# Kernel tuning notes

Measured on AMD Instinct MI355X. Metric: run time of the kernel, lower is better.

Reference implementation:

```python
import jax, jax.numpy as jnp
from jax import lax
import numpy as np


def _conv(x, w, b, stride=1, pad=0):
    # x: NCHW, w: OIHW
    o = lax.conv_general_dilated(x, w, (stride, stride), [(pad, pad), (pad, pad)],
                                 dimension_numbers=('NCHW', 'OIHW', 'NCHW'))
    return o + b[None, :, None, None]


def _up2(x):
    return jnp.repeat(jnp.repeat(x, 2, axis=2), 2, axis=3)


def _boundary_agg(x, w, b):
    # up_to_bottom = prefix-max along H; bottom_to_up = suffix-max along H;
    # left_to_right / right_to_left (via rot90) = prefix/suffix max along W (square spatial).
    x1 = lax.cummax(x, axis=2)
    x2 = lax.cummax(x, axis=2, reverse=True)
    x3 = lax.cummax(x, axis=3)
    x4 = lax.cummax(x, axis=3, reverse=True)
    return _conv(jnp.concatenate([x, x1, x2, x3, x4], axis=1), w, b)


def _forward(C3, C4, C5,
             ba3_w, ba3_b, ba4_w, ba4_b, ba5_w, ba5_b,
             p5_1_w, p5_1_b, p5_1d_w, p5_1d_b, p5_2_w, p5_2_b,
             p4_1_w, p4_1_b, p4_1d_w, p4_1d_b, p4_2_w, p4_2_b,
             p3_1_w, p3_1_b, p3_1d_w, p3_1d_b, p3_2_w, p3_2_b,
             p6_w, p6_b, p7_w, p7_b,
             c34_w, c34_b, c45_w, c45_b, c35_w, c35_b,
             gamma3, gamma4, gamma5):
    C3_BA = _boundary_agg(C3, ba3_w, ba3_b)
    C4_BA = _boundary_agg(C4, ba4_w, ba4_b)
    C5_BA = _boundary_agg(C5, ba5_w, ba5_b)
    # top-down path
    P5 = _conv(C5, p5_1_w, p5_1_b)
    P5u1 = _up2(P5)
    P5u2 = _up2(P5u1)
    P5 = _conv(P5, p5_2_w, p5_2_b, 1, 1)
    P4 = _conv(C4, p4_1_w, p4_1_b) + P5u1
    P4u1 = _up2(P4)
    P4 = _conv(P4, p4_2_w, p4_2_b, 1, 1)
    P3 = _conv(C3, p3_1_w, p3_1_b) + P4u1 + P5u2
    P3 = _conv(P3, p3_2_w, p3_2_b, 1, 1)
    # bottom-up (dual) path on boundary-aggregated features
    P3d = _conv(C3_BA, p3_1d_w, p3_1d_b)
    P3d1 = _conv(P3d, c34_w, c34_b, 2, 1)   # 3x3 s2 p1
    P3d2 = _conv(P3d1, c35_w, c35_b, 2, 0)  # 2x2 s2 p0
    P4d = _conv(C4_BA, p4_1d_w, p4_1d_b) + P3d1
    P4d1 = _conv(P4d, c45_w, c45_b, 2, 0)   # 2x2 s2 p0
    P5d = _conv(C5_BA, p5_1d_w, p5_1d_b) + P4d1 + P3d2
    # extra levels
    P6 = _conv(C5, p6_w, p6_b, 2, 1)
    P7 = _conv(jax.nn.relu(P6), p7_w, p7_b, 2, 1)
    # gated merge
    O3 = gamma3 * P3d + (1.0 - gamma3) * P3
    O4 = gamma4 * P4d + (1.0 - gamma4) * P4
    O5 = gamma5 * P5d + (1.0 - gamma5) * P5
    return (O3, O4, O5, P6, P7)


def setup_inputs() -> dict:
    key = jax.random.key(0)
    ks = iter(jax.random.split(key, 48))
    def rnd(shape, scale):
        return jax.random.normal(next(ks), shape, dtype=jnp.float32) * scale
    B, F = 8, 256
    d = {
        'C3': rnd((B, 256, 64, 64), 1.0),
        'C4': rnd((B, 512, 32, 32), 1.0),
        'C5': rnd((B, 1024, 16, 16), 1.0),
        # Boundary_Aggregation 1x1 convs: in_channels*5 -> in_channels
        'ba3_w': rnd((256, 1280, 1, 1), 0.02), 'ba3_b': rnd((256,), 0.02),
        'ba4_w': rnd((512, 2560, 1, 1), 0.02), 'ba4_b': rnd((512,), 0.02),
        'ba5_w': rnd((1024, 5120, 1, 1), 0.01), 'ba5_b': rnd((1024,), 0.02),
        # FPN lateral / smoothing convs
        'p5_1_w': rnd((F, 1024, 1, 1), 0.02), 'p5_1_b': rnd((F,), 0.02),
        'p5_1d_w': rnd((F, 1024, 1, 1), 0.02), 'p5_1d_b': rnd((F,), 0.02),
        'p5_2_w': rnd((F, F, 3, 3), 0.02), 'p5_2_b': rnd((F,), 0.02),
        'p4_1_w': rnd((F, 512, 1, 1), 0.02), 'p4_1_b': rnd((F,), 0.02),
        'p4_1d_w': rnd((F, 512, 1, 1), 0.02), 'p4_1d_b': rnd((F,), 0.02),
        'p4_2_w': rnd((F, F, 3, 3), 0.02), 'p4_2_b': rnd((F,), 0.02),
        'p3_1_w': rnd((F, 256, 1, 1), 0.02), 'p3_1_b': rnd((F,), 0.02),
        'p3_1d_w': rnd((F, 256, 1, 1), 0.02), 'p3_1d_b': rnd((F,), 0.02),
        'p3_2_w': rnd((F, F, 3, 3), 0.02), 'p3_2_b': rnd((F,), 0.02),
        'p6_w': rnd((F, 1024, 3, 3), 0.02), 'p6_b': rnd((F,), 0.02),
        'p7_w': rnd((F, F, 3, 3), 0.02), 'p7_b': rnd((F,), 0.02),
        # downsample convs in dual path
        'c34_w': rnd((F, F, 3, 3), 0.02), 'c34_b': rnd((F,), 0.02),
        'c45_w': rnd((F, F, 2, 2), 0.02), 'c45_b': rnd((F,), 0.02),
        'c35_w': rnd((F, F, 2, 2), 0.02), 'c35_b': rnd((F,), 0.02),
        'gamma3': rnd((1,), 0.3), 'gamma4': rnd((1,), 0.3), 'gamma5': rnd((1,), 0.3),
    }
    return d


def reference(C3, C4, C5,
              ba3_w, ba3_b, ba4_w, ba4_b, ba5_w, ba5_b,
              p5_1_w, p5_1_b, p5_1d_w, p5_1d_b, p5_2_w, p5_2_b,
              p4_1_w, p4_1_b, p4_1d_w, p4_1d_b, p4_2_w, p4_2_b,
              p3_1_w, p3_1_b, p3_1d_w, p3_1d_b, p3_2_w, p3_2_b,
              p6_w, p6_b, p7_w, p7_b,
              c34_w, c34_b, c45_w, c45_b, c35_w, c35_b,
              gamma3, gamma4, gamma5):
    return _forward(C3, C4, C5,
                    ba3_w, ba3_b, ba4_w, ba4_b, ba5_w, ba5_b,
                    p5_1_w, p5_1_b, p5_1d_w, p5_1d_b, p5_2_w, p5_2_b,
                    p4_1_w, p4_1_b, p4_1d_w, p4_1d_b, p4_2_w, p4_2_b,
                    p3_1_w, p3_1_b, p3_1d_w, p3_1d_b, p3_2_w, p3_2_b,
                    p6_w, p6_b, p7_w, p7_b,
                    c34_w, c34_b, c45_w, c45_b, c35_w, c35_b,
                    gamma3, gamma4, gamma5)
```

## Files before the change

### kernel.cpp

```cpp
#include <hip/hip_runtime.h>

typedef unsigned short u16;
typedef __attribute__((ext_vector_type(8))) short s8v;
typedef __attribute__((ext_vector_type(4))) float f4v;

__device__ __forceinline__ u16 f2bf(float f) {
  unsigned int x = __float_as_uint(f);
  return (u16)((x + 0x7fffu + ((x >> 16) & 1u)) >> 16);
}
__device__ __forceinline__ float bf2f(u16 u) {
  return __uint_as_float(((unsigned int)u) << 16);
}
__device__ __forceinline__ void gload16(const void* g, void* l) {
  __builtin_amdgcn_global_load_lds(
      (const __attribute__((address_space(1))) void*)g,
      (__attribute__((address_space(3))) void*)l, 16, 0, 0);
}

struct Epi {
  const float* bias;
  const u16* r1; int r1Hp, r1pad, r1sh;
  const u16* r2; int r2Hp, r2pad, r2sh;
  const float* gamma; const u16* other; int oHp, opad, gmode;
  u16* outB; int oBHp, oBpad, oBrelu;
  float* outF;
};

__device__ __forceinline__ size_t nhwc_idx(int b, int h, int w, int Hp, int pad, int Cc, int m) {
  return (((size_t)(b * Hp + h + pad)) * Hp + (w + pad)) * Cc + m;
}

__device__ __forceinline__ void epi4(f4v a, int mbase, int b, int oh, int ow,
                                     int p, int M, int l2ohow, float g, const Epi& ep) {
  float v[4];
#pragma unroll
  for (int r = 0; r < 4; ++r) v[r] = a[r];
  if (ep.bias) {
    const float* bp = &ep.bias[mbase];
#pragma unroll
    for (int r = 0; r < 4; ++r) v[r] += bp[r];
  }
  if (ep.r1) {
    const u16* rp = &ep.r1[nhwc_idx(b, oh >> ep.r1sh, ow >> ep.r1sh, ep.r1Hp, ep.r1pad, 256, mbase)];
#pragma unroll
    for (int r = 0; r < 4; ++r) v[r] += bf2f(rp[r]);
  }
  if (ep.r2) {
    const u16* rp = &ep.r2[nhwc_idx(b, oh >> ep.r2sh, ow >> ep.r2sh, ep.r2Hp, ep.r2pad, 256, mbase)];
#pragma unroll
    for (int r = 0; r < 4; ++r) v[r] += bf2f(rp[r]);
  }
  if (ep.gmode) {
    const u16* op = &ep.other[nhwc_idx(b, oh, ow, ep.oHp, ep.opad, 256, mbase)];
#pragma unroll
    for (int r = 0; r < 4; ++r) {
      float o = bf2f(op[r]);
      v[r] = (ep.gmode == 1) ? (g * o + (1.f - g) * v[r]) : (g * v[r] + (1.f - g) * o);
    }
  }
  if (ep.outF) {
    float* fp = &ep.outF[(((size_t)(b * M + mbase)) << l2ohow) + p];
#pragma unroll
    for (int r = 0; r < 4; ++r) fp[(size_t)r << l2ohow] = v[r];
  }
  if (ep.outB) {
    u16* obp = &ep.outB[nhwc_idx(b, oh, ow, ep.oBHp, ep.oBpad, M, mbase)];
    ushort4 pk;
    if (ep.oBrelu) { pk.x = f2bf(fmaxf(v[0], 0.f)); pk.y = f2bf(fmaxf(v[1], 0.f));
                     pk.z = f2bf(fmaxf(v[2], 0.f)); pk.w = f2bf(fmaxf(v[3], 0.f)); }
    else { pk.x = f2bf(v[0]); pk.y = f2bf(v[1]); pk.z = f2bf(v[2]); pk.w = f2bf(v[3]); }
    *(ushort4*)obp = pk;
  }
}

struct WSeg { const float* src; u16* dst; int K, l2Cin, mode, ktiles, blk0; };
struct WTab { WSeg s[17]; };

__global__ __launch_bounds__(256) void k_cvt_w(WTab tab) {
  int bid = blockIdx.x;
  int si = 0;
#pragma unroll
  for (int i = 1; i < 17; ++i) si += (bid >= tab.s[i].blk0) ? 1 : 0;
  WSeg sg = tab.s[si];
  int rel = bid - sg.blk0;
  int m = rel / sg.ktiles;
  int kt = rel - m * sg.ktiles;
  int r = kt * 256 + threadIdx.x;
  if (r >= sg.K) return;
  int Cin = 1 << sg.l2Cin;
  int q = r >> sg.l2Cin, c = r & (Cin - 1);
  int sidx;
  if (sg.mode == 1) {
    int og = (q < 4) ? (q + 1) : 0;
    sidx = m * sg.K + og * Cin + c;
  } else {
    int KHW = sg.K >> sg.l2Cin;
    sidx = (m * Cin + c) * KHW + q;
  }
  sg.dst[(size_t)m * sg.K + r] = f2bf(sg.src[sidx]);
}

__global__ __launch_bounds__(256) void k_cvt_x(const float* __restrict__ in, u16* __restrict__ out,
                                               int C, int H, int W, int Hp, int P, int tw) {
  __shared__ u16 tile[32][33];
  const int t = threadIdx.x;
  const int b = blockIdx.z, h = blockIdx.y;
  const int tc = blockIdx.x / tw, twi = blockIdx.x - tc * tw;
  const int c0 = tc * 32, w0 = twi * 32;
#pragma unroll
  for (int r = 0; r < 4; ++r) {
    int cl = (t >> 5) * 4 + r, wl = t & 31;
    if (w0 + wl < W) tile[cl][wl] = f2bf(in[(((size_t)b * C + c0 + cl) * H + h) * W + w0 + wl]);
  }
  __syncthreads();
#pragma unroll
  for (int r = 0; r < 4; ++r) {
    int wl = (t >> 5) * 4 + r, cl = t & 31;
    if (w0 + wl < W) out[(((size_t)(b * Hp + h + P)) * Hp + (w0 + wl + P)) * C + c0 + cl] = tile[cl][wl];
  }
}

template<int S, int L2S>
__global__ __launch_bounds__(256) void k_scan2(const float* __restrict__ x,
                                               u16* __restrict__ out, int l2C) {
  __shared__ u16 pl[S][S + 1], rp[S][S + 1], rs[S][S + 1];
  const int pid = blockIdx.x;
  const size_t SS = (size_t)S * S;
  const size_t GS = ((size_t)8 << l2C) * SS;
  const float* xp = x + (size_t)pid * SS;
  u16* g0 = out + (size_t)pid * SS;
  u16* g1 = g0 + GS;
  u16* g2 = g1 + GS;
  u16* g3 = g2 + GS;
  const int t = threadIdx.x;
  for (int idx = t; idx < S * S; idx += 256)
    pl[idx >> L2S][idx & (S - 1)] = f2bf(xp[idx]);
  __syncthreads();
  if (t < S) {
    float m = -INFINITY;
    for (int h = 0; h < S; ++h) { m = fmaxf(m, bf2f(pl[h][t])); g0[h * S + t] = f2bf(m); }
  } else if (t < 2 * S) {
    int c = t - S;
    float m = -INFINITY;
    for (int h = S - 1; h >= 0; --h) { m = fmaxf(m, bf2f(pl[h][c])); g1[h * S + c] = f2bf(m); }
  } else if (t < 3 * S) {
    int h = t - 2 * S;
    float m = -INFINITY;
    for (int w = 0; w < S; ++w) { m = fmaxf(m, bf2f(pl[h][w])); rp[h][w] = f2bf(m); }
  } else if (t < 4 * S) {
    int h = t - 3 * S;
    float m = -INFINITY;
    for (int w = S - 1; w >= 0; --w) { m = fmaxf(m, bf2f(pl[h][w])); rs[h][w] = f2bf(m); }
  }
  __syncthreads();
  for (int idx = t; idx < S * S; idx += 256) {
    g2[idx] = rp[idx >> L2S][idx & (S - 1)];
    g3[idx] = rs[idx >> L2S][idx & (S - 1)];
  }
}

__global__ __launch_bounds__(256) void k_tr(const u16* __restrict__ src, u16* __restrict__ dst,
                                            int C, int S, int tw) {
  __shared__ u16 tile[32][33];
  const int t = threadIdx.x;
  const int z = blockIdx.z, h = blockIdx.y;
  const int tc = blockIdx.x / tw, twi = blockIdx.x - tc * tw;
  const int c0 = tc * 32, w0 = twi * 32;
  const size_t SS = (size_t)S * S;
  const u16* sp = src + (size_t)z * C * SS;
  u16* dp = dst + (size_t)z * SS * C;
#pragma unroll
  for (int r = 0; r < 4; ++r) {
    int cl = (t >> 5) * 4 + r, wl = t & 31;
    if (w0 + wl < S) tile[cl][wl] = sp[(size_t)(c0 + cl) * SS + h * S + w0 + wl];
  }
  __syncthreads();
#pragma unroll
  for (int r = 0; r < 4; ++r) {
    int wl = (t >> 5) * 4 + r, cl = t & 31;
    if (w0 + wl < S) dp[((size_t)(h * S + w0 + wl)) * C + c0 + cl] = tile[cl][wl];
  }
}

template<int QDIV, int KW, int STR, bool FUSE>
__global__ __launch_bounds__(256)
void k_gemm(const u16* __restrict__ X, const u16* __restrict__ X2,
            const u16* __restrict__ Wt,
            float* __restrict__ part, int C, int l2C, int Hp, int ipad,
            int l2ohow, int l2ow, int K, int Ksp, int M, int N, Epi ep) {
  __shared__ u16 Al[4096];
  __shared__ u16 Bl[8192];
  const int tid = threadIdx.x, lane = tid & 63, wid = tid >> 6;

  int ntile, mtile;
  {
    const int NT = gridDim.x, MT = gridDim.y;
    int nm = blockIdx.x + NT * blockIdx.y;
    if ((NT & 7) == 0) {
      int low = nm & 7, r = nm >> 3;
      mtile = r % MT;
      ntile = ((r / MT) << 3) + low;
    } else { ntile = blockIdx.x; mtile = blockIdx.y; }
  }
  const int n0 = ntile * 128, m0 = mtile * 64;
  const int kb = blockIdx.z * Ksp;
  const int mw = (wid >> 1) * 32, nw = (wid & 1) * 64;

  const int srow = lane >> 2;
  const int schunk = (lane & 3) ^ ((srow >> 1) & 3);

  const u16* pa0 = Wt + (size_t)(m0 + wid * 16 + srow) * K + kb + schunk * 8;

  const u16* pb0 = nullptr; const u16* pb1 = nullptr;
  int rowB[2], ohsB[2], owsB[2];
  int q = 0, cnt = 0, khs = 0, kws = 0;
#pragma unroll
  for (int j = 0; j < 2; ++j) {
    int n = n0 + wid * 32 + j * 16 + srow;
    int b = n >> l2ohow, p = n & ((1 << l2ohow) - 1);
    int oh = p >> l2ow, ow = p & ((1 << l2ow) - 1);
    if (QDIV == 1) {
      const u16* gg = X + ((size_t)(b * Hp + oh + ipad) * Hp + (ow + ipad)) * C + kb + schunk * 8;
      if (j == 0) pb0 = gg; else pb1 = gg;
    } else if (QDIV == 5) {
      rowB[j] = n;
    } else {
      rowB[j] = b * Hp; ohsB[j] = oh * STR + ipad; owsB[j] = ow * STR + ipad;
    }
  }
  if (QDIV == 5) {
    q = kb >> l2C;
    int c0 = kb & (C - 1);
    cnt = (C - c0) >> 5;
    const u16* base = (q < 4) ? (X + (((size_t)q << Hp) << l2C)) : X2;
    pb0 = base + (((size_t)rowB[0]) << l2C) + c0 + schunk * 8;
    pb1 = base + (((size_t)rowB[1]) << l2C) + c0 + schunk * 8;
  } else if (QDIV != 1) {
    q = kb >> l2C;
    int c0 = kb & (C - 1);
    cnt = (C - c0) >> 5;
    if (QDIV == 4) { khs = q >> 1; kws = q & 1; } else { khs = q / 3; kws = q - khs * 3; }
    pb0 = X + ((size_t)(rowB[0] + ohsB[0] + khs) * Hp + (owsB[0] + kws)) * C + c0 + schunk * 8;
    pb1 = X + ((size_t)(rowB[1] + ohsB[1] + khs) * Hp + (owsB[1] + kws)) * C + c0 + schunk * 8;
  }

  f4v acc[2][4];
#pragma unroll
  for (int i = 0; i < 2; ++i)
#pragma unroll
    for (int j = 0; j < 4; ++j) acc[i][j] = (f4v){0.f, 0.f, 0.f, 0.f};

  const int fr = lane & 15, kc = lane >> 4;
  const int fxor = (kc ^ ((fr >> 1) & 3)) * 8;

  auto advB = [&]() {
    if (QDIV == 1) { pb0 += 32; pb1 += 32; }
    else if (--cnt == 0) {
      ++q; cnt = C >> 5;
      if (QDIV == 5) {
        const u16* base = (q < 4) ? (X + (((size_t)q << Hp) << l2C)) : X2;
        pb0 = base + (((size_t)rowB[0]) << l2C) + schunk * 8;
        pb1 = base + (((size_t)rowB[1]) << l2C) + schunk * 8;
      } else {
        if (++kws == KW) { kws = 0; ++khs; }
        pb0 = X + ((size_t)(rowB[0] + ohsB[0] + khs) * Hp + (owsB[0] + kws)) * C + schunk * 8;
        pb1 = X + ((size_t)(rowB[1] + ohsB[1] + khs) * Hp + (owsB[1] + kws)) * C + schunk * 8;
      }
    } else { pb0 += 32; pb1 += 32; }
  };
  auto stage = [&](int buf) {
    u16* la = Al + buf * 2048 + wid * 512;
    u16* lb = Bl + buf * 4096 + wid * 1024;
    gload16(pa0, la);
    gload16(pb0, lb); gload16(pb1, lb + 512);
    pa0 += 32;
    advB();
  };

  const int nt = Ksp >> 5;
  stage(0);
  for (int t = 0; t < nt; ++t) {
    const int cur = t & 1;
    if (t + 1 < nt) {
      stage(cur ^ 1);
      asm volatile("s_waitcnt vmcnt(3)" ::: "memory");
    } else {
      asm volatile("s_waitcnt vmcnt(0)" ::: "memory");
    }
    __builtin_amdgcn_s_barrier();
    asm volatile("" ::: "memory");
    const u16* ca = Al + cur * 2048;
    const u16* cb = Bl + cur * 4096;
    s8v a[2], bv[4];
#pragma unroll
    for (int mf = 0; mf < 2; ++mf) a[mf] = *(const s8v*)&ca[(mw + mf * 16 + fr) * 32 + fxor];
#pragma unroll
    for (int nf = 0; nf < 4; ++nf) bv[nf] = *(const s8v*)&cb[(nw + nf * 16 + fr) * 32 + fxor];
#pragma unroll
    for (int mf = 0; mf < 2; ++mf)
#pragma unroll
      for (int nf = 0; nf < 4; ++nf)
        acc[mf][nf] = __builtin_amdgcn_mfma_f32_16x16x32_bf16(a[mf], bv[nf], acc[mf][nf], 0, 0, 0);
    __builtin_amdgcn_s_barrier();
    asm volatile("" ::: "memory");
  }

  const int r4 = kc * 4;
  if (FUSE) {
    float g = ep.gmode ? *ep.gamma : 0.f;
#pragma unroll
    for (int nf = 0; nf < 4; ++nf) {
      int n = n0 + nw + nf * 16 + fr;
      int b = n >> l2ohow, p = n & ((1 << l2ohow) - 1);
      int oh = p >> l2ow, ow = p & ((1 << l2ow) - 1);
#pragma unroll
      for (int mf = 0; mf < 2; ++mf)
        epi4(acc[mf][nf], m0 + mw + mf * 16 + r4, b, oh, ow, p, M, l2ohow, g, ep);
    }
  } else {
#pragma unroll
    for (int nf = 0; nf < 4; ++nf) {
      int n = n0 + nw + nf * 16 + fr;
      float* pr = part + ((size_t)blockIdx.z * N + n) * M + m0 + mw + r4;
#pragma unroll
      for (int mf = 0; mf < 2; ++mf)
        *(f4v*)&pr[mf * 16] = acc[mf][nf];
    }
  }
}

__global__ __launch_bounds__(256)
void k_red2(const float* __restrict__ part, int z, int l2N, int l2M4, int M,
            int l2ohow, int l2ow, Epi ep) {
  const size_t total = (size_t)1 << (l2N + l2M4);
  const int N = 1 << l2N;
  float g = ep.gmode ? *ep.gamma : 0.f;
  for (size_t t = (size_t)blockIdx.x * 256 + threadIdx.x; t < total;
       t += (size_t)gridDim.x * 256) {
    int m4 = (int)(t & ((1u << l2M4) - 1));
    int n = (int)(t >> l2M4);
    int m = m4 << 2;
    f4v v = (f4v){0.f, 0.f, 0.f, 0.f};
    for (int s = 0; s < z; ++s) {
      f4v x = *(const f4v*)&part[((size_t)s * N + n) * M + m];
      v = v + x;
    }
    int b = n >> l2ohow, p = n & ((1 << l2ohow) - 1);
    int oh = p >> l2ow, ow = p & ((1 << l2ow) - 1);
    epi4(v, m, b, oh, ow, p, M, l2ohow, g, ep);
  }
}

static const size_t WR_BA3 = 0, WR_BA4 = 327680, WR_BA5 = 1638400,
  WR_P51 = 6881280, WR_P51D = 7143424, WR_P52 = 7405568, WR_P41 = 7995392,
  WR_P41D = 8126464, WR_P42 = 8257536, WR_P31 = 8847360, WR_P31D = 8912896,
  WR_P32 = 8978432, WR_P6 = 9568256, WR_P7 = 11927552, WR_C34 = 12517376,
  WR_C45 = 13107200, WR_C35 = 13369344;
static const size_t O_C3N = 13631488, O_C4N = 22020096, O_C5N = 26214400,
  O_C3BA = 28311552, O_C4BA = 36700160, O_C5BA = 40894464,
  O_CAT = 42991616, O_SCR = 76546048;
static const size_t O_P3D = O_CAT, O_P3PRE = O_CAT + 8921088,
  O_P4PRE = O_CAT + 17842176, O_P3D1 = O_CAT + 20209664,
  O_P4D = O_CAT + 22306816, O_P4D1 = O_CAT + 24403968,
  O_P3D2 = O_CAT + 24928256, O_P5PRE = O_CAT + 25452544,
  O_P5S = O_CAT + 26116096, O_P6R = O_CAT + 26640384, O_C5P = O_CAT + 26845184;

extern "C" void kernel_launch(void* const* d_in, const int* in_sizes, int n_in,
                              void* d_out, int out_size, void* d_ws, size_t ws_size,
                              hipStream_t stream) {
  (void)in_sizes; (void)n_in; (void)out_size; (void)ws_size;
  const float* C3 = (const float*)d_in[0];
  const float* C4 = (const float*)d_in[1];
  const float* C5 = (const float*)d_in[2];
  const float* ba3_w = (const float*)d_in[3];  const float* ba3_b = (const float*)d_in[4];
  const float* ba4_w = (const float*)d_in[5];  const float* ba4_b = (const float*)d_in[6];
  const float* ba5_w = (const float*)d_in[7];  const float* ba5_b = (const float*)d_in[8];
  const float* p5_1_w = (const float*)d_in[9];  const float* p5_1_b = (const float*)d_in[10];
  const float* p5_1d_w = (const float*)d_in[11]; const float* p5_1d_b = (const float*)d_in[12];
  const float* p5_2_w = (const float*)d_in[13]; const float* p5_2_b = (const float*)d_in[14];
  const float* p4_1_w = (const float*)d_in[15]; const float* p4_1_b = (const float*)d_in[16];
  const float* p4_1d_w = (const float*)d_in[17]; const float* p4_1d_b = (const float*)d_in[18];
  const float* p4_2_w = (const float*)d_in[19]; const float* p4_2_b = (const float*)d_in[20];
  const float* p3_1_w = (const float*)d_in[21]; const float* p3_1_b = (const float*)d_in[22];
  const float* p3_1d_w = (const float*)d_in[23]; const float* p3_1d_b = (const float*)d_in[24];
  const float* p3_2_w = (const float*)d_in[25]; const float* p3_2_b = (const float*)d_in[26];
  const float* p6_w = (const float*)d_in[27]; const float* p6_b = (const float*)d_in[28];
  const float* p7_w = (const float*)d_in[29]; const float* p7_b = (const float*)d_in[30];
  const float* c34_w = (const float*)d_in[31]; const float* c34_b = (const float*)d_in[32];
  const float* c45_w = (const float*)d_in[33]; const float* c45_b = (const float*)d_in[34];
  const float* c35_w = (const float*)d_in[35]; const float* c35_b = (const float*)d_in[36];
  const float* g3 = (const float*)d_in[37];
  const float* g4 = (const float*)d_in[38];
  const float* g5 = (const float*)d_in[39];

  float* out = (float*)d_out;
  float* O3 = out;
  float* O4 = out + 8388608;
  float* O5 = out + 10485760;
  float* P6o = out + 11010048;
  float* P7o = out + 11141120;

  u16* wsu = (u16*)d_ws;
  u16* c3n = wsu + O_C3N;  u16* c4n = wsu + O_C4N;  u16* c5n = wsu + O_C5N;
  u16* c3ba = wsu + O_C3BA; u16* c4ba = wsu + O_C4BA; u16* c5ba = wsu + O_C5BA;
  u16* catb = wsu + O_CAT;
  u16* scr = wsu + O_SCR;
  u16* p3d = wsu + O_P3D;  u16* p3d1 = wsu + O_P3D1; u16* p3d2 = wsu + O_P3D2;
  u16* p4d = wsu + O_P4D;  u16* p4d1 = wsu + O_P4D1;
  u16* p5pre = wsu + O_P5PRE; u16* p5s = wsu + O_P5S; u16* p4pre = wsu + O_P4PRE;
  u16* p3pre = wsu + O_P3PRE; u16* p6r = wsu + O_P6R; u16* c5p = wsu + O_C5P;
  float* part = (float*)scr;
  float* partba = (float*)scr;

  const Epi enone = {nullptr, nullptr,0,0,0, nullptr,0,0,0, nullptr,nullptr,0,0,0, nullptr,0,0,0, nullptr};

  WTab tab;
  int ti = 0, blk = 0;
  auto add = [&](const float* s, size_t off, int M, int K, int l2Cin, int mode) {
    int kt = (K + 255) / 256;
    tab.s[ti].src = s; tab.s[ti].dst = wsu + off; tab.s[ti].K = K;
    tab.s[ti].l2Cin = l2Cin; tab.s[ti].mode = mode;
    tab.s[ti].ktiles = kt; tab.s[ti].blk0 = blk;
    blk += M * kt; ++ti;
  };
  add(ba3_w, WR_BA3, 256, 1280, 8, 1);
  add(ba4_w, WR_BA4, 512, 2560, 9, 1);
  add(ba5_w, WR_BA5, 1024, 5120, 10, 1);
  add(p5_1_w, WR_P51, 256, 1024, 10, 0);
  add(p5_1d_w, WR_P51D, 256, 1024, 10, 0);
  add(p5_2_w, WR_P52, 256, 2304, 8, 0);
  add(p4_1_w, WR_P41, 256, 512, 9, 0);
  add(p4_1d_w, WR_P41D, 256, 512, 9, 0);
  add(p4_2_w, WR_P42, 256, 2304, 8, 0);
  add(p3_1_w, WR_P31, 256, 256, 8, 0);
  add(p3_1d_w, WR_P31D, 256, 256, 8, 0);
  add(p3_2_w, WR_P32, 256, 2304, 8, 0);
  add(p6_w, WR_P6, 256, 9216, 10, 0);
  add(p7_w, WR_P7, 256, 2304, 8, 0);
  add(c34_w, WR_C34, 256, 2304, 8, 0);
  add(c45_w, WR_C45, 256, 1024, 8, 0);
  add(c35_w, WR_C35, 256, 1024, 8, 0);
  k_cvt_w<<<blk, 256, 0, stream>>>(tab);

  k_cvt_x<<<dim3(16,64,8), 256, 0, stream>>>(C3, c3n, 256, 64, 64, 64, 0, 2);
  k_cvt_x<<<dim3(16,32,8), 256, 0, stream>>>(C4, c4n, 512, 32, 32, 32, 0, 1);
  k_cvt_x<<<dim3(32,16,8), 256, 0, stream>>>(C5, c5n, 1024, 16, 16, 16, 0, 1);

  k_scan2<64, 6><<<2048, 256, 0, stream>>>(C3, scr, 8);
  k_tr<<<dim3(16,64,32), 256, 0, stream>>>(scr, catb, 256, 64, 2);
  {
    Epi ep = {ba3_b, nullptr,0,0,0, nullptr,0,0,0, nullptr,nullptr,0,0,0, c3ba,64,0,0, nullptr};
    k_gemm<5,1,1,true><<<dim3(256,4,1), 256, 0, stream>>>(
        catb, c3n, wsu + WR_BA3, nullptr, 256, 8, 15, 0, 12, 6, 1280, 1280, 256, 32768, ep);
  }
  k_scan2<32, 5><<<4096, 256, 0, stream>>>(C4, scr, 9);
  k_tr<<<dim3(16,32,32), 256, 0, stream>>>(scr, catb, 512, 32, 1);
  k_gemm<5,1,1,false><<<dim3(64,8,2), 256, 0, stream>>>(
      catb, c4n, wsu + WR_BA4, partba, 512, 9, 13, 0, 10, 5, 2560, 1280, 512, 8192, enone);
  {
    Epi ep = {ba4_b, nullptr,0,0,0, nullptr,0,0,0, nullptr,nullptr,0,0,0, c4ba,32,0,0, nullptr};
    k_red2<<<2048, 256, 0, stream>>>(partba, 2, 13, 7, 512, 10, 5, ep);
  }
  k_scan2<16, 4><<<8192, 256, 0, stream>>>(C5, scr, 10);
  k_tr<<<dim3(32,16,32), 256, 0, stream>>>(scr, catb, 1024, 16, 1);
  k_gemm<5,1,1,false><<<dim3(16,16,4), 256, 0, stream>>>(
      catb, c5n, wsu + WR_BA5, partba, 1024, 10, 11, 0, 8, 4, 5120, 1280, 1024, 2048, enone);
  {
    Epi ep = {ba5_b, nullptr,0,0,0, nullptr,0,0,0, nullptr,nullptr,0,0,0, c5ba,16,0,0, nullptr};
    k_red2<<<2048, 256, 0, stream>>>(partba, 4, 11, 8, 1024, 8, 4, ep);
  }

  hipMemsetAsync(p3d, 0, (size_t)8921088 * 2, stream);
  hipMemsetAsync(p3pre, 0, (size_t)8921088 * 2, stream);
  hipMemsetAsync(p4pre, 0, (size_t)2367488 * 2, stream);
  hipMemsetAsync(p5pre, 0, (size_t)663552 * 2, stream);
  hipMemsetAsync(p6r, 0, (size_t)204800 * 2, stream);
  hipMemsetAsync(c5p, 0, (size_t)2654208 * 2, stream);
  k_cvt_x<<<dim3(32,16,8), 256, 0, stream>>>(C5, c5p, 1024, 16, 16, 18, 1, 1);

  {
    Epi ep = {p3_1d_b, nullptr,0,0,0, nullptr,0,0,0, nullptr,nullptr,0,0,0, p3d,66,1,0, nullptr};
    k_gemm<1,1,1,true><<<dim3(256,4,1), 256, 0, stream>>>(
        c3ba, nullptr, wsu + WR_P31D, nullptr, 256, 0, 64, 0, 12, 6, 256, 256, 256, 32768, ep);
  }
  k_gemm<9,3,2,false><<<dim3(64,4,4), 256, 0, stream>>>(
      p3d, nullptr, wsu + WR_C34, part, 256, 8, 66, 0, 10, 5, 2304, 576, 256, 8192, enone);
  {
    Epi ep = {c34_b, nullptr,0,0,0, nullptr,0,0,0, nullptr,nullptr,0,0,0, p3d1,32,0,0, nullptr};
    k_red2<<<2048, 256, 0, stream>>>(part, 4, 13, 6, 256, 10, 5, ep);
  }
  k_gemm<4,2,2,false><<<dim3(16,4,8), 256, 0, stream>>>(
      p3d1, nullptr, wsu + WR_C35, part, 256, 8, 32, 0, 8, 4, 1024, 128, 256, 2048, enone);
  {
    Epi ep = {c35_b, nullptr,0,0,0, nullptr,0,0,0, nullptr,nullptr,0,0,0, p3d2,16,0,0, nullptr};
    k_red2<<<2048, 256, 0, stream>>>(part, 8, 11, 6, 256, 8, 4, ep);
  }
  k_gemm<1,1,1,false><<<dim3(64,4,4), 256, 0, stream>>>(
      c4ba, nullptr, wsu + WR_P41D, part, 512, 0, 32, 0, 10, 5, 512, 128, 256, 8192, enone);
  {
    Epi ep = {p4_1d_b, p3d1,32,0,0, nullptr,0,0,0, nullptr,nullptr,0,0,0, p4d,32,0,0, nullptr};
    k_red2<<<2048, 256, 0, stream>>>(part, 4, 13, 6, 256, 10, 5, ep);
  }
  k_gemm<4,2,2,false><<<dim3(16,4,8), 256, 0, stream>>>(
      p4d, nullptr, wsu + WR_C45, part, 256, 8, 32, 0, 8, 4, 1024, 128, 256, 2048, enone);
  {
    Epi ep = {c45_b, nullptr,0,0,0, nullptr,0,0,0, nullptr,nullptr,0,0,0, p4d1,16,0,0, nullptr};
    k_red2<<<2048, 256, 0, stream>>>(part, 8, 11, 6, 256, 8, 4, ep);
  }

  k_gemm<1,1,1,false><<<dim3(16,4,8), 256, 0, stream>>>(
      c5n, nullptr, wsu + WR_P51, part, 1024, 0, 16, 0, 8, 4, 1024, 128, 256, 2048, enone);
  {
    Epi ep = {p5_1_b, nullptr,0,0,0, nullptr,0,0,0, nullptr,nullptr,0,0,0, p5pre,18,1,0, nullptr};
    k_red2<<<2048, 256, 0, stream>>>(part, 8, 11, 6, 256, 8, 4, ep);
  }
  k_gemm<9,3,1,false><<<dim3(16,4,8), 256, 0, stream>>>(
      p5pre, nullptr, wsu + WR_P52, part, 256, 8, 18, 0, 8, 4, 2304, 288, 256, 2048, enone);
  {
    Epi ep = {p5_2_b, nullptr,0,0,0, nullptr,0,0,0, nullptr,nullptr,0,0,0, p5s,16,0,0, nullptr};
    k_red2<<<2048, 256, 0, stream>>>(part, 8, 11, 6, 256, 8, 4, ep);
  }
  k_gemm<1,1,1,false><<<dim3(64,4,4), 256, 0, stream>>>(
      c4n, nullptr, wsu + WR_P41, part, 512, 0, 32, 0, 10, 5, 512, 128, 256, 8192, enone);
  {
    Epi ep = {p4_1_b, p5pre,18,1,1, nullptr,0,0,0, nullptr,nullptr,0,0,0, p4pre,34,1,0, nullptr};
    k_red2<<<2048, 256, 0, stream>>>(part, 4, 13, 6, 256, 10, 5, ep);
  }
  k_gemm<9,3,1,false><<<dim3(64,4,4), 256, 0, stream>>>(
      p4pre, nullptr, wsu + WR_P42, part, 256, 8, 34, 0, 10, 5, 2304, 576, 256, 8192, enone);
  {
    Epi ep = {p4_2_b, nullptr,0,0,0, nullptr,0,0,0, g4,p4d,32,0,1, nullptr,0,0,0, O4};
    k_red2<<<2048, 256, 0, stream>>>(part, 4, 13, 6, 256, 10, 5, ep);
  }
  {
    Epi ep = {p3_1_b, p4pre,34,1,1, p5pre,18,1,2, nullptr,nullptr,0,0,0, p3pre,66,1,0, nullptr};
    k_gemm<1,1,1,true><<<dim3(256,4,1), 256, 0, stream>>>(
        c3n, nullptr, wsu + WR_P31, nullptr, 256, 0, 64, 0, 12, 6, 256, 256, 256, 32768, ep);
  }
  {
    Epi ep = {p3_2_b, nullptr,0,0,0, nullptr,0,0,0, g3,p3d,66,1,1, nullptr,0,0,0, O3};
    k_gemm<9,3,1,true><<<dim3(256,4,1), 256, 0, stream>>>(
        p3pre, nullptr, wsu + WR_P32, nullptr, 256, 8, 66, 0, 12, 6, 2304, 2304, 256, 32768, ep);
  }
  k_gemm<1,1,1,false><<<dim3(16,4,8), 256, 0, stream>>>(
      c5ba, nullptr, wsu + WR_P51D, part, 1024, 0, 16, 0, 8, 4, 1024, 128, 256, 2048, enone);
  {
    Epi ep = {p5_1d_b, p4d1,16,0,0, p3d2,16,0,0, g5,p5s,16,0,2, nullptr,0,0,0, O5};
    k_red2<<<2048, 256, 0, stream>>>(part, 8, 11, 6, 256, 8, 4, ep);
  }

  k_gemm<9,3,2,false><<<dim3(4,4,32), 256, 0, stream>>>(
      c5p, nullptr, wsu + WR_P6, part, 1024, 10, 18, 0, 6, 3, 9216, 288, 256, 512, enone);
  {
    Epi ep = {p6_b, nullptr,0,0,0, nullptr,0,0,0, nullptr,nullptr,0,0,0, p6r,10,1,1, P6o};
    k_red2<<<512, 256, 0, stream>>>(part, 32, 9, 6, 256, 6, 3, ep);
  }
  k_gemm<9,3,2,false><<<dim3(1,4,8), 256, 0, stream>>>(
      p6r, nullptr, wsu + WR_P7, part, 256, 8, 10, 0, 4, 2, 2304, 288, 256, 128, enone);
  {
    Epi ep = {p7_b, nullptr,0,0,0, nullptr,0,0,0, nullptr,nullptr,0,0,0, nullptr,0,0,0, P7o};
    k_red2<<<128, 256, 0, stream>>>(part, 8, 7, 6, 256, 4, 2, ep);
  }
}
```

Measured before the change: 716.7 us.

## Scan cummax directly on NHWC bf16 input, removing scratch transpose pass

After: 665.4 us. 1.08x faster.

```diff
diff --git a/kernel.cpp b/kernel.cpp
--- a/kernel.cpp
+++ b/kernel.cpp
@@ -120,65 +120,67 @@
   }
 }
 
-template<int S, int L2S>
-__global__ __launch_bounds__(256) void k_scan2(const float* __restrict__ x,
-                                               u16* __restrict__ out, int l2C) {
-  __shared__ u16 pl[S][S + 1], rp[S][S + 1], rs[S][S + 1];
-  const int pid = blockIdx.x;
-  const size_t SS = (size_t)S * S;
-  const size_t GS = ((size_t)8 << l2C) * SS;
-  const float* xp = x + (size_t)pid * SS;
-  u16* g0 = out + (size_t)pid * SS;
-  u16* g1 = g0 + GS;
-  u16* g2 = g1 + GS;
-  u16* g3 = g2 + GS;
+__global__ __launch_bounds__(256)
+void k_scanH(const u16* __restrict__ in, u16* __restrict__ out0, u16* __restrict__ out1,
+             int S, int C) {
+  const int cpw = C >> 2;
+  const int wpb = 256 / cpw;
+  const int strips = S / wpb;
   const int t = threadIdx.x;
-  for (int idx = t; idx < S * S; idx += 256)
-    pl[idx >> L2S][idx & (S - 1)] = f2bf(xp[idx]);
-  __syncthreads();
-  if (t < S) {
-    float m = -INFINITY;
-    for (int h = 0; h < S; ++h) { m = fmaxf(m, bf2f(pl[h][t])); g0[h * S + t] = f2bf(m); }
-  } else if (t < 2 * S) {
-    int c = t - S;
-    float m = -INFINITY;
-    for (int h = S - 1; h >= 0; --h) { m = fmaxf(m, bf2f(pl[h][c])); g1[h * S + c] = f2bf(m); }
-  } else if (t < 3 * S) {
-    int h = t - 2 * S;
-    float m = -INFINITY;
-    for (int w = 0; w < S; ++w) { m = fmaxf(m, bf2f(pl[h][w])); rp[h][w] = f2bf(m); }
-  } else if (t < 4 * S) {
-    int h = t - 3 * S;
-    float m = -INFINITY;
-    for (int w = S - 1; w >= 0; --w) { m = fmaxf(m, bf2f(pl[h][w])); rs[h][w] = f2bf(m); }
-  }
-  __syncthreads();
-  for (int idx = t; idx < S * S; idx += 256) {
-    g2[idx] = rp[idx >> L2S][idx & (S - 1)];
-    g3[idx] = rs[idx >> L2S][idx & (S - 1)];
-  }
-}
-
-__global__ __launch_bounds__(256) void k_tr(const u16* __restrict__ src, u16* __restrict__ dst,
-                                            int C, int S, int tw) {
-  __shared__ u16 tile[32][33];
+  const int wl = t / cpw, c4 = t - wl * cpw;
+  const int bb = blockIdx.x / strips, strip = blockIdx.x - bb * strips;
+  const int w = strip * wpb + wl;
+  const size_t hstr = (size_t)S * C;
+  const size_t base = (((size_t)bb * S) * S + w) * C + c4 * 4;
+  float m0 = -INFINITY, m1 = -INFINITY, m2 = -INFINITY, m3 = -INFINITY;
+  if (blockIdx.y == 0) {
+    for (int h = 0; h < S; ++h) {
+      ushort4 v = *(const ushort4*)&in[base + (size_t)h * hstr];
+      m0 = fmaxf(m0, bf2f(v.x)); m1 = fmaxf(m1, bf2f(v.y));
+      m2 = fmaxf(m2, bf2f(v.z)); m3 = fmaxf(m3, bf2f(v.w));
+      ushort4 o; o.x = f2bf(m0); o.y = f2bf(m1); o.z = f2bf(m2); o.w = f2bf(m3);
+      *(ushort4*)&out0[base + (size_t)h * hstr] = o;
+    }
+  } else {
+    for (int h = S - 1; h >= 0; --h) {
+      ushort4 v = *(const ushort4*)&in[base + (size_t)h * hstr];
+      m0 = fmaxf(m0, bf2f(v.x)); m1 = fmaxf(m1, bf2f(v.y));
+      m2 = fmaxf(m2, bf2f(v.z)); m3 = fmaxf(m3, bf2f(v.w));
+      ushort4 o; o.x = f2bf(m0); o.y = f2bf(m1); o.z = f2bf(m2); o.w = f2bf(m3);
+      *(ushort4*)&out1[base + (size_t)h * hstr] = o;
+    }
+  }
+}
+
+__global__ __launch_bounds__(256)
+void k_scanW(const u16* __restrict__ in, u16* __restrict__ out0, u16* __restrict__ out1,
+             int S, int C) {
+  const int cph = C >> 2;
+  const int hpb = 256 / cph;
+  const int strips = S / hpb;
   const int t = threadIdx.x;
-  const int z = blockIdx.z, h = blockIdx.y;
-  const int tc = blockIdx.x / tw, twi = blockIdx.x - tc * tw;
-  const int c0 = tc * 32, w0 = twi * 32;
-  const size_t SS = (size_t)S * S;
-  const u16* sp = src + (size_t)z * C * SS;
-  u16* dp = dst + (size_t)z * SS * C;
-#pragma unroll
-  for (int r = 0; r < 4; ++r) {
-    int cl = (t >> 5) * 4 + r, wl = t & 31;
-    if (w0 + wl < S) tile[cl][wl] = sp[(size_t)(c0 + cl) * SS + h * S + w0 + wl];
-  }
-  __syncthreads();
-#pragma unroll
-  for (int r = 0; r < 4; ++r) {
-    int wl = (t >> 5) * 4 + r, cl = t & 31;
-    if (w0 + wl < S) dp[((size_t)(h * S + w0 + wl)) * C + c0 + cl] = tile[cl][wl];
+  const int hl = t / cph, c4 = t - hl * cph;
+  const int bb = blockIdx.x / strips, strip = blockIdx.x - bb * strips;
+  const int h = strip * hpb + hl;
+  const size_t wstr = (size_t)C;
+  const size_t base = (((size_t)bb * S + h) * S) * C + c4 * 4;
+  float m0 = -INFINITY, m1 = -INFINITY, m2 = -INFINITY, m3 = -INFINITY;
+  if (blockIdx.y == 0) {
+    for (int w = 0; w < S; ++w) {
+      ushort4 v = *(const ushort4*)&in[base + (size_t)w * wstr];
+      m0 = fmaxf(m0, bf2f(v.x)); m1 = fmaxf(m1, bf2f(v.y));
+      m2 = fmaxf(m2, bf2f(v.z)); m3 = fmaxf(m3, bf2f(v.w));
+      ushort4 o; o.x = f2bf(m0); o.y = f2bf(m1); o.z = f2bf(m2); o.w = f2bf(m3);
+      *(ushort4*)&out0[base + (size_t)w * wstr] = o;
+    }
+  } else {
+    for (int w = S - 1; w >= 0; --w) {
+      ushort4 v = *(const ushort4*)&in[base + (size_t)w * wstr];
+      m0 = fmaxf(m0, bf2f(v.x)); m1 = fmaxf(m1, bf2f(v.y));
+      m2 = fmaxf(m2, bf2f(v.z)); m3 = fmaxf(m3, bf2f(v.w));
+      ushort4 o; o.x = f2bf(m0); o.y = f2bf(m1); o.z = f2bf(m2); o.w = f2bf(m3);
+      *(ushort4*)&out1[base + (size_t)w * wstr] = o;
+    }
   }
 }
 
@@ -446,26 +448,29 @@
   k_cvt_x<<<dim3(16,32,8), 256, 0, stream>>>(C4, c4n, 512, 32, 32, 32, 0, 1);
   k_cvt_x<<<dim3(32,16,8), 256, 0, stream>>>(C5, c5n, 1024, 16, 16, 16, 0, 1);
 
-  k_scan2<64, 6><<<2048, 256, 0, stream>>>(C3, scr, 8);
-  k_tr<<<dim3(16,64,32), 256, 0, stream>>>(scr, catb, 256, 64, 2);
-  {
+  {
+    const size_t GS3 = 8388608;
+    k_scanH<<<dim3(128,2), 256, 0, stream>>>(c3n, catb, catb + GS3, 64, 256);
+    k_scanW<<<dim3(128,2), 256, 0, stream>>>(c3n, catb + 2*GS3, catb + 3*GS3, 64, 256);
     Epi ep = {ba3_b, nullptr,0,0,0, nullptr,0,0,0, nullptr,nullptr,0,0,0, c3ba,64,0,0, nullptr};
     k_gemm<5,1,1,true><<<dim3(256,4,1), 256, 0, stream>>>(
         catb, c3n, wsu + WR_BA3, nullptr, 256, 8, 15, 0, 12, 6, 1280, 1280, 256, 32768, ep);
   }
-  k_scan2<32, 5><<<4096, 256, 0, stream>>>(C4, scr, 9);
-  k_tr<<<dim3(16,32,32), 256, 0, stream>>>(scr, catb, 512, 32, 1);
-  k_gemm<5,1,1,false><<<dim3(64,8,2), 256, 0, stream>>>(
-      catb, c4n, wsu + WR_BA4, partba, 512, 9, 13, 0, 10, 5, 2560, 1280, 512, 8192, enone);
-  {
+  {
+    const size_t GS4 = 4194304;
+    k_scanH<<<dim3(128,2), 256, 0, stream>>>(c4n, catb, catb + GS4, 32, 512);
+    k_scanW<<<dim3(128,2), 256, 0, stream>>>(c4n, catb + 2*GS4, catb + 3*GS4, 32, 512);
+    k_gemm<5,1,1,false><<<dim3(64,8,2), 256, 0, stream>>>(
+        catb, c4n, wsu + WR_BA4, partba, 512, 9, 13, 0, 10, 5, 2560, 1280, 512, 8192, enone);
     Epi ep = {ba4_b, nullptr,0,0,0, nullptr,0,0,0, nullptr,nullptr,0,0,0, c4ba,32,0,0, nullptr};
     k_red2<<<2048, 256, 0, stream>>>(partba, 2, 13, 7, 512, 10, 5, ep);
   }
-  k_scan2<16, 4><<<8192, 256, 0, stream>>>(C5, scr, 10);
-  k_tr<<<dim3(32,16,32), 256, 0, stream>>>(scr, catb, 1024, 16, 1);
-  k_gemm<5,1,1,false><<<dim3(16,16,4), 256, 0, stream>>>(
-      catb, c5n, wsu + WR_BA5, partba, 1024, 10, 11, 0, 8, 4, 5120, 1280, 1024, 2048, enone);
-  {
+  {
+    const size_t GS5 = 2097152;
+    k_scanH<<<dim3(128,2), 256, 0, stream>>>(c5n, catb, catb + GS5, 16, 1024);
+    k_scanW<<<dim3(128,2), 256, 0, stream>>>(c5n, catb + 2*GS5, catb + 3*GS5, 16, 1024);
+    k_gemm<5,1,1,false><<<dim3(16,16,4), 256, 0, stream>>>(
+        catb, c5n, wsu + WR_BA5, partba, 1024, 10, 11, 0, 8, 4, 5120, 1280, 1024, 2048, enone);
     Epi ep = {ba5_b, nullptr,0,0,0, nullptr,0,0,0, nullptr,nullptr,0,0,0, c5ba,16,0,0, nullptr};
     k_red2<<<2048, 256, 0, stream>>>(partba, 4, 11, 8, 1024, 8, 4, ep);
   }
```
